# Optimization experiments

Measured on AMD Instinct MI355X. Metric: run time of the kernel, lower is better.

The kernel has to match this reference:

```python
import jax, jax.numpy as jnp
import numpy as np

B, L, D, H, UNITS = 64, 4096, 512, 512, 256

def setup_inputs() -> dict:
    key = jax.random.key(0)
    ks = jax.random.split(key, 8)
    s = lambda fan_in: 1.0 / np.sqrt(fan_in)
    return {
        "features": jax.random.normal(ks[0], (B, L, D), dtype=jnp.float32),
        "hidden": jax.random.normal(ks[1], (B, H), dtype=jnp.float32),
        "W1_k": jax.random.uniform(ks[2], (D, UNITS), jnp.float32, -s(D), s(D)),
        "W1_b": jnp.zeros((UNITS,), jnp.float32),
        "W2_k": jax.random.uniform(ks[3], (H, UNITS), jnp.float32, -s(H), s(H)),
        "W2_b": jnp.zeros((UNITS,), jnp.float32),
        "V_k": jax.random.uniform(ks[4], (UNITS, 1), jnp.float32, -s(UNITS), s(UNITS)),
        "V_b": jnp.zeros((1,), jnp.float32),
    }

def reference(features, hidden, W1_k, W1_b, W2_k, W2_b, V_k, V_b):
    # features: [B, L, D], hidden: [B, H]
    f_proj = jnp.einsum('bld,du->blu', features, W1_k) + W1_b          # [B, L, U]
    h_proj = (hidden @ W2_k + W2_b)[:, None, :]                        # [B, 1, U]
    score = jnp.einsum('blu,uo->blo', jnp.tanh(f_proj + h_proj), V_k) + V_b  # [B, L, 1]
    attention_weights = jax.nn.softmax(score, axis=1)                  # [B, L, 1]
    context_vector = jnp.sum(attention_weights * features, axis=1)     # [B, D]
    return (context_vector, attention_weights)
```

## Files before the change

### kernel.cpp

```cpp
#include <hip/hip_runtime.h>

#define Bsz 64
#define Lsz 4096
#define Dsz 512
#define Hsz 512
#define Usz 256
#define LT  64
#define NLB (Lsz / LT)

typedef __attribute__((ext_vector_type(8))) short s8v;
typedef __attribute__((ext_vector_type(4))) float f4v;
typedef __attribute__((ext_vector_type(8))) unsigned short u16x8;

#define SW(r, c) (((((c) >> 3) ^ ((r) & 7)) << 3) | ((c) & 7))

__device__ __forceinline__ unsigned short f2bf(float f) {
    unsigned int u = __float_as_uint(f);
    u += 0x7FFFu + ((u >> 16) & 1u);
    return (unsigned short)(u >> 16);
}
__device__ __forceinline__ float bf2f(unsigned int lo16) {
    return __uint_as_float(lo16 << 16);
}
__device__ __forceinline__ void barrier_lds() {
    asm volatile("s_waitcnt lgkmcnt(0)" ::: "memory");
    __builtin_amdgcn_s_barrier();
}


__global__ __launch_bounds__(256) void k_prep(const float* __restrict__ W1,
                                              const float* __restrict__ hidden,
                                              const float* __restrict__ W2,
                                              unsigned short* __restrict__ W1Tf,
                                              float* __restrict__ hp_part,
                                              float* __restrict__ den,
                                              float* __restrict__ ctx_acc) {
    int blk = blockIdx.x, tid = threadIdx.x;
    if (blk < 32) {
        __shared__ unsigned short Lt[64][72];
        int kb = blk >> 2, ub = blk & 3;
        {
            int rr = tid >> 2, c16 = (tid & 3) * 16;
            const float* src = W1 + (size_t)(kb * 64 + rr) * Usz + ub * 64 + c16;
            f4v v0 = *reinterpret_cast<const f4v*>(src);
            f4v v1 = *reinterpret_cast<const f4v*>(src + 4);
            f4v v2 = *reinterpret_cast<const f4v*>(src + 8);
            f4v v3 = *reinterpret_cast<const f4v*>(src + 12);
            u16x8 o0 = { f2bf(v0.x), f2bf(v0.y), f2bf(v0.z), f2bf(v0.w),
                         f2bf(v1.x), f2bf(v1.y), f2bf(v1.z), f2bf(v1.w) };
            u16x8 o1 = { f2bf(v2.x), f2bf(v2.y), f2bf(v2.z), f2bf(v2.w),
                         f2bf(v3.x), f2bf(v3.y), f2bf(v3.z), f2bf(v3.w) };
            *reinterpret_cast<u16x8*>(&Lt[rr][c16])     = o0;
            *reinterpret_cast<u16x8*>(&Lt[rr][c16 + 8]) = o1;
        }
        __syncthreads();
        {
            int ur = tid >> 2, k16 = (tid & 3) * 16;
            u16x8 o0, o1;
#pragma unroll
            for (int i = 0; i < 8; ++i) o0[i] = Lt[k16 + i][ur];
#pragma unroll
            for (int i = 0; i < 8; ++i) o1[i] = Lt[k16 + 8 + i][ur];
            const int kb32 = kb * 2 + (k16 >> 5);
            const int lg0  = (k16 >> 3) & 3;
            const int cg   = ub * 4 + (ur >> 4);
            const int lr   = ur & 15;
            unsigned short* d0 = W1Tf + ((size_t)(kb32 * 16 + cg) * 512) + (lg0 * 16 + lr) * 8;
            unsigned short* d1 = W1Tf + ((size_t)(kb32 * 16 + cg) * 512) + ((lg0 + 1) * 16 + lr) * 8;
            *reinterpret_cast<u16x8*>(d0) = o0;
            *reinterpret_cast<u16x8*>(d1) = o1;
        }
    } else if (blk < 288) {
        int idx = blk - 32;
        int kq = idx >> 6, b = idx & 63;
        const float* hrow = hidden + (size_t)b * Hsz + kq * 128;
        const float* w2p  = W2 + (size_t)(kq * 128) * Usz + tid;
        float a0 = 0.f, a1 = 0.f, a2 = 0.f, a3 = 0.f;
#pragma unroll 8
        for (int k = 0; k < 128; k += 4) {
            a0 = fmaf(hrow[k + 0], w2p[(size_t)(k + 0) * Usz], a0);
            a1 = fmaf(hrow[k + 1], w2p[(size_t)(k + 1) * Usz], a1);
            a2 = fmaf(hrow[k + 2], w2p[(size_t)(k + 2) * Usz], a2);
            a3 = fmaf(hrow[k + 3], w2p[(size_t)(k + 3) * Usz], a3);
        }
        hp_part[((size_t)kq * Bsz + b) * Usz + tid] = (a0 + a1) + (a2 + a3);
    } else {
        int b = blk - 288;
        if (tid == 0) den[b] = 0.f;
        ctx_acc[b * Dsz + tid] = 0.f;
        ctx_acc[b * Dsz + 256 + tid] = 0.f;
    }
}

__global__ void __launch_bounds__(512)
__attribute__((amdgpu_waves_per_eu(4, 4))) k_score_ctx(
    const float* __restrict__ feat, const unsigned short* __restrict__ W1Tf,
    const float* __restrict__ hp_part, const float* __restrict__ W1b,
    const float* __restrict__ W2b, const float* __restrict__ Vk,
    const float* __restrict__ Vb, float* __restrict__ el_arr,
    float* __restrict__ den, float* __restrict__ ctx_acc)
{
    __shared__ __align__(16) unsigned short A[LT][Dsz];
    __shared__ float hp[Usz], vv[Usz];
    __shared__ float spart[8][LT];
    __shared__ float el[LT];
    __shared__ float pc[2][Dsz];

    const int tid  = threadIdx.x;
    const int w    = tid >> 6;
    const int lane = tid & 63;
    const int lr   = lane & 15;
    const int lg   = lane >> 4;
    const int b    = blockIdx.x >> 6;
    const int lb   = blockIdx.x & 63;
    const int l0   = lb * LT;

    const int srow = tid >> 3;
    const int sfc  = (tid & 7) * 16;
    const float* fb = feat + ((size_t)b * Lsz + l0 + srow) * Dsz + sfc;

    f4v st[2][4];
#pragma unroll
    for (int i = 0; i < 4; ++i) st[0][i] = *reinterpret_cast<const f4v*>(fb + i * 4);
#pragma unroll
    for (int i = 0; i < 4; ++i) st[1][i] = *reinterpret_cast<const f4v*>(fb + 128 + i * 4);
    __builtin_amdgcn_sched_barrier(0);

    if (tid < Usz) {
        const float* hpb = hp_part + (size_t)b * Usz + tid;
        hp[tid] = (hpb[0] + hpb[Bsz * Usz]) + (hpb[2 * Bsz * Usz] + hpb[3 * Bsz * Usz])
                + W1b[tid] + W2b[tid];
        vv[tid] = Vk[tid];
    }
    {
        u16x8 o0 = { f2bf(st[0][0].x), f2bf(st[0][0].y), f2bf(st[0][0].z), f2bf(st[0][0].w),
                     f2bf(st[0][1].x), f2bf(st[0][1].y), f2bf(st[0][1].z), f2bf(st[0][1].w) };
        u16x8 o1 = { f2bf(st[0][2].x), f2bf(st[0][2].y), f2bf(st[0][2].z), f2bf(st[0][2].w),
                     f2bf(st[0][3].x), f2bf(st[0][3].y), f2bf(st[0][3].z), f2bf(st[0][3].w) };
        *reinterpret_cast<u16x8*>(&A[srow][SW(srow, sfc)])     = o0;
        *reinterpret_cast<u16x8*>(&A[srow][SW(srow, sfc + 8)]) = o1;
    }
    barrier_lds();

    const unsigned short* bpf = W1Tf + (size_t)(w * 2) * 512 + lane * 8;
    f4v acc[4][2];
#pragma unroll
    for (int mf = 0; mf < 4; ++mf) {
        acc[mf][0] = (f4v){0.f, 0.f, 0.f, 0.f};
        acc[mf][1] = (f4v){0.f, 0.f, 0.f, 0.f};
    }

#pragma unroll
    for (int c = 0; c < 4; ++c) {
        s8v bq[4][2];
#pragma unroll
        for (int k = 0; k < 4; ++k) {
            const size_t kbo = (size_t)((c * 4 + k) * 16) * 512;
            bq[k][0] = *reinterpret_cast<const s8v*>(bpf + kbo);
            bq[k][1] = *reinterpret_cast<const s8v*>(bpf + kbo + 512);
        }
        __builtin_amdgcn_sched_barrier(0);
        if (c < 2) {
#pragma unroll
            for (int i = 0; i < 4; ++i)
                st[c & 1][i] = *reinterpret_cast<const f4v*>(fb + (c + 2) * 128 + i * 4);
        }
        __builtin_amdgcn_sched_barrier(0);
#pragma unroll
        for (int k = 0; k < 4; ++k) {
            const int kof = (c * 4 + k) * 32 + lg * 8;
#pragma unroll
            for (int mf = 0; mf < 4; ++mf) {
                const int row = mf * 16 + lr;
                s8v a = *reinterpret_cast<const s8v*>(&A[row][SW(row, kof)]);
                acc[mf][0] = __builtin_amdgcn_mfma_f32_16x16x32_bf16(a, bq[k][0], acc[mf][0], 0, 0, 0);
                acc[mf][1] = __builtin_amdgcn_mfma_f32_16x16x32_bf16(a, bq[k][1], acc[mf][1], 0, 0, 0);
            }
        }
        __builtin_amdgcn_sched_barrier(0);
        if (c < 3) {
            const int cc = (c + 1) * 128 + sfc;
            const f4v* s = st[(c + 1) & 1];
            u16x8 o0 = { f2bf(s[0].x), f2bf(s[0].y), f2bf(s[0].z), f2bf(s[0].w),
                         f2bf(s[1].x), f2bf(s[1].y), f2bf(s[1].z), f2bf(s[1].w) };
            u16x8 o1 = { f2bf(s[2].x), f2bf(s[2].y), f2bf(s[2].z), f2bf(s[2].w),
                         f2bf(s[3].x), f2bf(s[3].y), f2bf(s[3].z), f2bf(s[3].w) };
            *reinterpret_cast<u16x8*>(&A[srow][SW(srow, cc)])     = o0;
            *reinterpret_cast<u16x8*>(&A[srow][SW(srow, cc + 8)]) = o1;
            barrier_lds();
        }
    }

    {
        float rs[4][4];
#pragma unroll
        for (int mf = 0; mf < 4; ++mf)
#pragma unroll
            for (int r = 0; r < 4; ++r) rs[mf][r] = 0.f;
#pragma unroll
        for (int mf = 0; mf < 4; ++mf)
#pragma unroll
            for (int nf = 0; nf < 2; ++nf) {
                int col = w * 32 + nf * 16 + lr;
                float hpv = hp[col], vvv = vv[col];
#pragma unroll
                for (int r = 0; r < 4; ++r) {
                    float x = acc[mf][nf][r] + hpv;
                    float e = __expf(2.f * x);
                    rs[mf][r] = fmaf(1.f - 2.f / (e + 1.f), vvv, rs[mf][r]);
                }
            }
#pragma unroll
        for (int off = 1; off < 16; off <<= 1)
#pragma unroll
            for (int mf = 0; mf < 4; ++mf)
#pragma unroll
                for (int r = 0; r < 4; ++r)
                    rs[mf][r] += __shfl_xor(rs[mf][r], off, 64);
        if (lr == 0)
#pragma unroll
            for (int mf = 0; mf < 4; ++mf)
#pragma unroll
                for (int r = 0; r < 4; ++r)
                    spart[w][mf * 16 + lg * 4 + r] = rs[mf][r];
    }
    barrier_lds();

    if (tid < LT) {
        float s = Vb[0];
#pragma unroll
        for (int ww = 0; ww < 8; ++ww) s += spart[ww][tid];
        float e = __expf(s);
        el[tid] = e;
        el_arr[(size_t)b * Lsz + l0 + tid] = e;
        float es = e;
#pragma unroll
        for (int off = 1; off < 64; off <<= 1) es += __shfl_xor(es, off, 64);
        if (tid == 0) atomicAdd(&den[b], es);
    }
    barrier_lds();

    {
        const int qr = tid >> 8;
        const int d0 = (tid & 255) * 2;
        float a0 = 0.f, a1 = 0.f;
#pragma unroll 8
        for (int li = 0; li < 32; ++li) {
            int l = qr * 32 + li;
            unsigned int pk = *reinterpret_cast<const unsigned int*>(&A[l][SW(l, d0)]);
            float e = el[l];
            a0 = fmaf(e, bf2f(pk & 0xFFFFu), a0);
            a1 = fmaf(e, bf2f(pk >> 16), a1);
        }
        pc[qr][d0]     = a0;
        pc[qr][d0 + 1] = a1;
    }
    barrier_lds();
    atomicAdd(&ctx_acc[b * Dsz + tid], pc[0][tid] + pc[1][tid]);
}

__global__ __launch_bounds__(256) void k_finalize(const float* __restrict__ el_arr,
                                                  const float* __restrict__ den,
                                                  const float* __restrict__ ctx_acc,
                                                  float* __restrict__ ctx,
                                                  float* __restrict__ wout) {
    int blk = blockIdx.x, tid = threadIdx.x;
    int b = blk >> 2, q = blk & 3;
    float inv = 1.f / den[b];
    size_t base = (size_t)b * Lsz + q * 1024 + tid * 4;
    f4v e4 = *reinterpret_cast<const f4v*>(&el_arr[base]);
    f4v w4 = { e4.x * inv, e4.y * inv, e4.z * inv, e4.w * inv };
    *reinterpret_cast<f4v*>(&wout[base]) = w4;
    if (tid < 128) {
        int d = q * 128 + tid;
        ctx[(size_t)b * Dsz + d] = ctx_acc[b * Dsz + d] * inv;
    }
}

extern "C" void kernel_launch(void* const* d_in, const int* in_sizes, int n_in,
                              void* d_out, int out_size, void* d_ws, size_t ws_size,
                              hipStream_t stream) {
    const float* feat   = (const float*)d_in[0];
    const float* hidden = (const float*)d_in[1];
    const float* W1     = (const float*)d_in[2];
    const float* W1b    = (const float*)d_in[3];
    const float* W2     = (const float*)d_in[4];
    const float* W2b    = (const float*)d_in[5];
    const float* Vk     = (const float*)d_in[6];
    const float* Vb     = (const float*)d_in[7];

    unsigned short* w1tf = (unsigned short*)d_ws;
    float* hp_part = (float*)((char*)d_ws + 256 * 1024);
    float* el_arr  = (float*)((char*)d_ws + 512 * 1024);
    float* den     = (float*)((char*)d_ws + 1536 * 1024);
    float* ctx_acc = (float*)((char*)d_ws + 1536 * 1024 + 256);

    float* ctx  = (float*)d_out;
    float* wout = ctx + Bsz * Dsz;

    k_prep<<<352, 256, 0, stream>>>(W1, hidden, W2, w1tf, hp_part, den, ctx_acc);
    k_score_ctx<<<Bsz * NLB, 512, 0, stream>>>(feat, w1tf, hp_part, W1b, W2b,
                                               Vk, Vb, el_arr, den, ctx_acc);
    k_finalize<<<Bsz * 4, 256, 0, stream>>>(el_arr, den, ctx_acc, ctx, wout);
}
```

Before: 163.9 us.

## Halve L tile to 32 rows and double waves per EU for occupancy

Shrinks the per-block sequence tile from 64 to 32 rows, doubling the grid and halving the LDS tile, and raises the waves-per-EU hint from 4 to 8 so more blocks can be resident at once. The in-loop overlap of feature loads with MFMA is replaced: all four feature chunks are now converted to bf16 and staged into LDS before the matmul starts, and the MFMA loop is regrouped into smaller batches of W1 fragment loads. Intent is to hide memory latency through occupancy instead of software pipelining. The cost is that each W1 fragment is reused over half as many rows, so W1 is re-read from cache twice as often, and den/ctx atomics double.

```diff
diff --git a/kernel.cpp b/kernel.cpp
--- a/kernel.cpp
+++ b/kernel.cpp
@@ -5,7 +5,7 @@
 #define Dsz 512
 #define Hsz 512
 #define Usz 256
-#define LT  64
+#define LT  32
 #define NLB (Lsz / LT)
 
 typedef __attribute__((ext_vector_type(8))) short s8v;
@@ -93,7 +93,7 @@
 }
 
 __global__ void __launch_bounds__(512)
-__attribute__((amdgpu_waves_per_eu(4, 4))) k_score_ctx(
+__attribute__((amdgpu_waves_per_eu(8, 8))) k_score_ctx(
     const float* __restrict__ feat, const unsigned short* __restrict__ W1Tf,
     const float* __restrict__ hp_part, const float* __restrict__ W1b,
     const float* __restrict__ W2b, const float* __restrict__ Vk,
@@ -111,19 +111,19 @@
     const int lane = tid & 63;
     const int lr   = lane & 15;
     const int lg   = lane >> 4;
-    const int b    = blockIdx.x >> 6;
-    const int lb   = blockIdx.x & 63;
+    const int b    = blockIdx.x >> 7;
+    const int lb   = blockIdx.x & 127;
     const int l0   = lb * LT;
 
-    const int srow = tid >> 3;
-    const int sfc  = (tid & 7) * 16;
+    const int srow = tid >> 4;
+    const int sfc  = (tid & 15) * 8;
     const float* fb = feat + ((size_t)b * Lsz + l0 + srow) * Dsz + sfc;
 
-    f4v st[2][4];
-#pragma unroll
-    for (int i = 0; i < 4; ++i) st[0][i] = *reinterpret_cast<const f4v*>(fb + i * 4);
-#pragma unroll
-    for (int i = 0; i < 4; ++i) st[1][i] = *reinterpret_cast<const f4v*>(fb + 128 + i * 4);
+    f4v st[2][2];
+    st[0][0] = *reinterpret_cast<const f4v*>(fb);
+    st[0][1] = *reinterpret_cast<const f4v*>(fb + 4);
+    st[1][0] = *reinterpret_cast<const f4v*>(fb + 128);
+    st[1][1] = *reinterpret_cast<const f4v*>(fb + 132);
     __builtin_amdgcn_sched_barrier(0);
 
     if (tid < Usz) {
@@ -132,73 +132,65 @@
                 + W1b[tid] + W2b[tid];
         vv[tid] = Vk[tid];
     }
+
+#pragma unroll
+    for (int c = 0; c < 4; ++c) {
+        {
+            const f4v* s = st[c & 1];
+            const int cc = c * 128 + sfc;
+            u16x8 o = { f2bf(s[0].x), f2bf(s[0].y), f2bf(s[0].z), f2bf(s[0].w),
+                        f2bf(s[1].x), f2bf(s[1].y), f2bf(s[1].z), f2bf(s[1].w) };
+            *reinterpret_cast<u16x8*>(&A[srow][SW(srow, cc)]) = o;
+        }
+        if (c < 2) {
+            st[c & 1][0] = *reinterpret_cast<const f4v*>(fb + (c + 2) * 128);
+            st[c & 1][1] = *reinterpret_cast<const f4v*>(fb + (c + 2) * 128 + 4);
+        }
+        __builtin_amdgcn_sched_barrier(0);
+    }
+    barrier_lds();
+
+    const unsigned short* bpf = W1Tf + (size_t)(w * 2) * 512 + lane * 8;
+    f4v acc[2][2];
+    acc[0][0] = (f4v){0.f, 0.f, 0.f, 0.f};
+    acc[0][1] = (f4v){0.f, 0.f, 0.f, 0.f};
+    acc[1][0] = (f4v){0.f, 0.f, 0.f, 0.f};
+    acc[1][1] = (f4v){0.f, 0.f, 0.f, 0.f};
+
+#pragma unroll
+    for (int c = 0; c < 4; ++c) {
+#pragma unroll
+        for (int g = 0; g < 2; ++g) {
+            s8v bq[2][2];
+#pragma unroll
+            for (int k = 0; k < 2; ++k) {
+                const size_t kbo = (size_t)((c * 4 + g * 2 + k) * 16) * 512;
+                bq[k][0] = *reinterpret_cast<const s8v*>(bpf + kbo);
+                bq[k][1] = *reinterpret_cast<const s8v*>(bpf + kbo + 512);
+            }
+            __builtin_amdgcn_sched_barrier(0);
+#pragma unroll
+            for (int k = 0; k < 2; ++k) {
+                const int kof = (c * 4 + g * 2 + k) * 32 + lg * 8;
+#pragma unroll
+                for (int mf = 0; mf < 2; ++mf) {
+                    const int row = mf * 16 + lr;
+                    s8v a = *reinterpret_cast<const s8v*>(&A[row][SW(row, kof)]);
+                    acc[mf][0] = __builtin_amdgcn_mfma_f32_16x16x32_bf16(a, bq[k][0], acc[mf][0], 0, 0, 0);
+                    acc[mf][1] = __builtin_amdgcn_mfma_f32_16x16x32_bf16(a, bq[k][1], acc[mf][1], 0, 0, 0);
+                }
+            }
+        }
+    }
+
     {
-        u16x8 o0 = { f2bf(st[0][0].x), f2bf(st[0][0].y), f2bf(st[0][0].z), f2bf(st[0][0].w),
-                     f2bf(st[0][1].x), f2bf(st[0][1].y), f2bf(st[0][1].z), f2bf(st[0][1].w) };
-        u16x8 o1 = { f2bf(st[0][2].x), f2bf(st[0][2].y), f2bf(st[0][2].z), f2bf(st[0][2].w),
-                     f2bf(st[0][3].x), f2bf(st[0][3].y), f2bf(st[0][3].z), f2bf(st[0][3].w) };
-        *reinterpret_cast<u16x8*>(&A[srow][SW(srow, sfc)])     = o0;
-        *reinterpret_cast<u16x8*>(&A[srow][SW(srow, sfc + 8)]) = o1;
-    }
-    barrier_lds();
-
-    const unsigned short* bpf = W1Tf + (size_t)(w * 2) * 512 + lane * 8;
-    f4v acc[4][2];
-#pragma unroll
-    for (int mf = 0; mf < 4; ++mf) {
-        acc[mf][0] = (f4v){0.f, 0.f, 0.f, 0.f};
-        acc[mf][1] = (f4v){0.f, 0.f, 0.f, 0.f};
-    }
-
-#pragma unroll
-    for (int c = 0; c < 4; ++c) {
-        s8v bq[4][2];
-#pragma unroll
-        for (int k = 0; k < 4; ++k) {
-            const size_t kbo = (size_t)((c * 4 + k) * 16) * 512;
-            bq[k][0] = *reinterpret_cast<const s8v*>(bpf + kbo);
-            bq[k][1] = *reinterpret_cast<const s8v*>(bpf + kbo + 512);
-        }
-        __builtin_amdgcn_sched_barrier(0);
-        if (c < 2) {
-#pragma unroll
-            for (int i = 0; i < 4; ++i)
-                st[c & 1][i] = *reinterpret_cast<const f4v*>(fb + (c + 2) * 128 + i * 4);
-        }
-        __builtin_amdgcn_sched_barrier(0);
-#pragma unroll
-        for (int k = 0; k < 4; ++k) {
-            const int kof = (c * 4 + k) * 32 + lg * 8;
-#pragma unroll
-            for (int mf = 0; mf < 4; ++mf) {
-                const int row = mf * 16 + lr;
-                s8v a = *reinterpret_cast<const s8v*>(&A[row][SW(row, kof)]);
-                acc[mf][0] = __builtin_amdgcn_mfma_f32_16x16x32_bf16(a, bq[k][0], acc[mf][0], 0, 0, 0);
-                acc[mf][1] = __builtin_amdgcn_mfma_f32_16x16x32_bf16(a, bq[k][1], acc[mf][1], 0, 0, 0);
-            }
-        }
-        __builtin_amdgcn_sched_barrier(0);
-        if (c < 3) {
-            const int cc = (c + 1) * 128 + sfc;
-            const f4v* s = st[(c + 1) & 1];
-            u16x8 o0 = { f2bf(s[0].x), f2bf(s[0].y), f2bf(s[0].z), f2bf(s[0].w),
-                         f2bf(s[1].x), f2bf(s[1].y), f2bf(s[1].z), f2bf(s[1].w) };
-            u16x8 o1 = { f2bf(s[2].x), f2bf(s[2].y), f2bf(s[2].z), f2bf(s[2].w),
-                         f2bf(s[3].x), f2bf(s[3].y), f2bf(s[3].z), f2bf(s[3].w) };
-            *reinterpret_cast<u16x8*>(&A[srow][SW(srow, cc)])     = o0;
-            *reinterpret_cast<u16x8*>(&A[srow][SW(srow, cc + 8)]) = o1;
-            barrier_lds();
-        }
-    }
-
-    {
-        float rs[4][4];
-#pragma unroll
-        for (int mf = 0; mf < 4; ++mf)
+        float rs[2][4];
+#pragma unroll
+        for (int mf = 0; mf < 2; ++mf)
 #pragma unroll
             for (int r = 0; r < 4; ++r) rs[mf][r] = 0.f;
 #pragma unroll
-        for (int mf = 0; mf < 4; ++mf)
+        for (int mf = 0; mf < 2; ++mf)
 #pragma unroll
             for (int nf = 0; nf < 2; ++nf) {
                 int col = w * 32 + nf * 16 + lr;
@@ -213,13 +205,13 @@
 #pragma unroll
         for (int off = 1; off < 16; off <<= 1)
 #pragma unroll
-            for (int mf = 0; mf < 4; ++mf)
+            for (int mf = 0; mf < 2; ++mf)
 #pragma unroll
                 for (int r = 0; r < 4; ++r)
                     rs[mf][r] += __shfl_xor(rs[mf][r], off, 64);
         if (lr == 0)
 #pragma unroll
-            for (int mf = 0; mf < 4; ++mf)
+            for (int mf = 0; mf < 2; ++mf)
 #pragma unroll
                 for (int r = 0; r < 4; ++r)
                     spart[w][mf * 16 + lg * 4 + r] = rs[mf][r];
@@ -235,7 +227,7 @@
         el_arr[(size_t)b * Lsz + l0 + tid] = e;
         float es = e;
 #pragma unroll
-        for (int off = 1; off < 64; off <<= 1) es += __shfl_xor(es, off, 64);
+        for (int off = 1; off < 32; off <<= 1) es += __shfl_xor(es, off, 64);
         if (tid == 0) atomicAdd(&den[b], es);
     }
     barrier_lds();
@@ -244,9 +236,9 @@
         const int qr = tid >> 8;
         const int d0 = (tid & 255) * 2;
         float a0 = 0.f, a1 = 0.f;
-#pragma unroll 8
-        for (int li = 0; li < 32; ++li) {
-            int l = qr * 32 + li;
+#pragma unroll
+        for (int li = 0; li < 16; ++li) {
+            int l = qr * 16 + li;
             unsigned int pk = *reinterpret_cast<const unsigned int*>(&A[l][SW(l, d0)]);
             float e = el[l];
             a0 = fmaf(e, bf2f(pk & 0xFFFFu), a0);
```

Measured after the change: 178.5 us. +8.9%, slower.
